# Kernel optimization log

Hardware: AMD Instinct MI355X
Metric: run time of the kernel (lower is better)

## Reference

```python
import jax, jax.numpy as jnp
import numpy as np

DEPTH = 8            # max(code_depth)
CODE_DEPTH = (1, 8)  # (vqgan_depth, vqkd_depth)
N_EMBED = 8192
EMBED_DIM = 64
B, H, W = 32, 32, 32


def setup_inputs() -> dict:
    key = jax.random.key(0)
    kx, kc = jax.random.split(key)
    x = jax.random.normal(kx, (B, EMBED_DIM, H, W), dtype=jnp.float32)
    # 8 codebooks, each (n_embed, embed_dim); torch nn.Embedding init is N(0,1)
    codebooks = jax.random.normal(kc, (DEPTH, N_EMBED, EMBED_DIM), dtype=jnp.float32)
    return {"x": x, "codebooks": codebooks}


def _quantize(x_code, codebooks):
    # x_code: (B, h, w, d) -- already stop-gradient'd (torch clones a detached copy)
    b, h, w, d = x_code.shape
    xf = x_code.reshape(-1, d)  # (N, d)

    def step(carry, cb):
        residual, agg = carry
        # squared L2 distances via ||r||^2 + ||c||^2 - 2 r c^T  (torch addmm)
        r_sq = jnp.sum(residual * residual, axis=1, keepdims=True)      # (N, 1)
        c_sq = jnp.sum(cb * cb, axis=1)[None, :]                         # (1, K)
        dist = r_sq + c_sq - 2.0 * (residual @ cb.T)                     # (N, K)
        code = jnp.argmin(dist, axis=1)                                  # (N,)
        quant = cb[code]                                                 # (N, d)
        d_norm = jnp.mean(jnp.sum(dist * dist, axis=-1))
        residual = residual - quant
        agg = agg + quant
        return (residual, agg), (agg, code, d_norm)

    (_, _), (quants, codes, d_norms) = jax.lax.scan(
        step, (xf, jnp.zeros_like(xf)), codebooks)
    quants = quants.reshape(DEPTH, b, h, w, d)             # cumulative quants
    codes = jnp.transpose(codes.reshape(DEPTH, b, h, w), (1, 2, 3, 0))  # (B,h,w,DEPTH)
    return quants, codes, d_norms


def reference(x, codebooks):
    x_code = jnp.transpose(x, (0, 2, 3, 1))  # b c h w -> b h w c
    quants, codes, d_norms = _quantize(jax.lax.stop_gradient(x_code), codebooks)
    # commitment loss: mean over depth of mean((x - agg_quant.detach())^2)
    commit_loss = jnp.mean((x_code[None] - jax.lax.stop_gradient(quants)) ** 2)
    # straight-through outputs in latent (b c h w) shape
    vqkd = jnp.transpose(quants[CODE_DEPTH[1] - 1], (0, 3, 1, 2))
    vqkd_zq = x + jax.lax.stop_gradient(vqkd - x)
    vqgan = jnp.transpose(quants[CODE_DEPTH[0] - 1], (0, 3, 1, 2))
    vqgan_zq = x + jax.lax.stop_gradient(vqgan - x)
    vqkd_d_norm = d_norms[CODE_DEPTH[1] - 1]
    vqgan_d_norm = d_norms[CODE_DEPTH[0] - 1]
    return (vqgan_zq, vqkd_zq, commit_loss, vqkd_d_norm, vqgan_d_norm, codes)
```

## Files before the change

kernel.cpp:

```cpp
#include <hip/hip_runtime.h>

#define OFF_RES    0u
#define OFF_BH     8388608u
#define OFF_BL     9437184u
#define OFF_CSQD   10485760u
#define OFF_CSQH   11010048u
#define OFF_CODES  11272192u
#define OFF_PM1    11403264u
#define OFF_PM2    12451840u
#define OFF_PI1    13500416u
#define OFF_FLAG   14548992u
#define OFF_M0     14680064u
#define OFF_M7     14712832u
#define OFF_DNP    14745600u
#define OFF_ACC    14749696u
#define OFF_PCOM   14749760u
#define OFF_PDN    15274048u

#define TAU 3.0e-3f

typedef __attribute__((ext_vector_type(8))) _Float16 f16x8;
typedef __attribute__((ext_vector_type(4))) float f32x4;

__device__ __forceinline__ f32x4 mfma16(f16x8 a, f16x8 b, f32x4 c) {
  return __builtin_amdgcn_mfma_f32_16x16x32_f16(a, b, c, 0, 0, 0);
}

__global__ __launch_bounds__(256) void srq_transpose_init(
    const float* __restrict__ x, float* __restrict__ resid)
{
  __shared__ float tile[64][65];
  const int b   = blockIdx.x >> 4;
  const int hw0 = (blockIdx.x & 15) << 6;
  const int t = threadIdx.x;
#pragma unroll
  for (int i = 0; i < 16; ++i) {
    int e = i * 256 + t;
    int c = e >> 6, hw = e & 63;
    tile[c][hw] = x[(size_t)b * 65536 + (size_t)c * 1024 + hw0 + hw];
  }
  __syncthreads();
#pragma unroll
  for (int i = 0; i < 16; ++i) {
    int e = i * 256 + t;
    int hw = e >> 6, c = e & 63;
    resid[((size_t)(b * 1024 + hw0 + hw) << 6) + c] = tile[c][hw];
  }
}

__global__ __launch_bounds__(256) void srq_csq(
    const float* __restrict__ cb, double* __restrict__ csqD, float* __restrict__ csqH)
{
  int id = blockIdx.x * 256 + threadIdx.x;
  const float* p = cb + ((size_t)id << 6);
  double s = 0.0;
#pragma unroll 8
  for (int d = 0; d < 64; ++d) { double v = (double)p[d]; s = fma(v, v, s); }
  csqD[id] = s;
  csqH[id] = (float)(-0.5 * s);
}

__global__ __launch_bounds__(256) void srq_bconv(
    const float* __restrict__ cb, _Float16* __restrict__ Bh, _Float16* __restrict__ Bl)
{
  int id = blockIdx.x * 256 + threadIdx.x;
  float v = cb[id];
  _Float16 h = (_Float16)v;
  Bh[id] = h;
  Bl[id] = (_Float16)((v - (float)h) * 2048.f);
}

__global__ __launch_bounds__(256) void srq_dnpre_partial(
    const float* __restrict__ cb, const double* __restrict__ csqD,
    double* __restrict__ Pm, double* __restrict__ Ps1, double* __restrict__ Ps2)
{
  __shared__ float ch[32][64];
  const int t = threadIdx.x;
  const int b = blockIdx.x;
  const int i = t >> 2;
  const int j0 = (t & 3) << 4;
  double acc[16];
#pragma unroll
  for (int n = 0; n < 16; ++n) acc[n] = 0.0;
  double s1 = 0.0, s2 = 0.0;
  for (int c8 = 0; c8 < 8; ++c8) {
    const int kbase = b * 256 + c8 * 32;
    __syncthreads();
    const float* src = cb + (size_t)kbase * 64;
#pragma unroll
    for (int u = 0; u < 2; ++u)
      *(float4*)(&ch[0][0] + (u * 256 + t) * 4) = *(const float4*)(src + (u * 256 + t) * 4);
    __syncthreads();
#pragma unroll 4
    for (int kk = 0; kk < 32; ++kk) {
      double ci = (double)ch[kk][i];
#pragma unroll
      for (int n = 0; n < 16; ++n)
        acc[n] = fma(ci, (double)ch[kk][j0 + n], acc[n]);
    }
    if (t < 64) {
#pragma unroll 4
      for (int kk = 0; kk < 32; ++kk) {
        double v = (double)ch[kk][t];
        s1 += v;
        s2 = fma(csqD[kbase + kk], v, s2);
      }
    }
  }
  double* dst = Pm + ((size_t)b << 12) + (i << 6) + j0;
#pragma unroll
  for (int n = 0; n < 16; ++n) dst[n] = acc[n];
  if (t < 64) { Ps1[(b << 6) + t] = s1; Ps2[(b << 6) + t] = s2; }
}

__global__ __launch_bounds__(256) void srq_dnpre_reduce(
    const double* __restrict__ Pm, const double* __restrict__ Ps1,
    const double* __restrict__ Ps2, const double* __restrict__ csqD,
    double* __restrict__ Mmat, double* __restrict__ S1, double* __restrict__ S2,
    double* __restrict__ CS)
{
  const int t = threadIdx.x;
  if (blockIdx.x < 16) {
    const int e = blockIdx.x * 256 + t;
    double a = 0.0;
    for (int b = 0; b < 32; ++b) a += Pm[((size_t)b << 12) + e];
    Mmat[e] = a;
  } else {
    __shared__ double red[256];
    if (t < 64) {
      double a1 = 0.0, a2 = 0.0;
      for (int b = 0; b < 32; ++b) { a1 += Ps1[(b << 6) + t]; a2 += Ps2[(b << 6) + t]; }
      S1[t] = a1; S2[t] = a2;
    }
    double c1 = 0.0, c2 = 0.0;
    for (int k = t; k < 8192; k += 256) { double q = csqD[k]; c1 += q; c2 = fma(q, q, c2); }
    red[t] = c1;
    __syncthreads();
    for (int o = 128; o; o >>= 1) { if (t < o) red[t] += red[t + o]; __syncthreads(); }
    if (t == 0) CS[0] = red[0];
    __syncthreads();
    red[t] = c2;
    __syncthreads();
    for (int o = 128; o; o >>= 1) { if (t < o) red[t] += red[t + o]; __syncthreads(); }
    if (t == 0) CS[1] = red[0];
  }
}

__device__ __forceinline__ void stage_tile(
    const _Float16* __restrict__ Bh, const _Float16* __restrict__ Bl,
    char* ldsbase, int k0, int wid, int lane)
{
#pragma unroll
  for (int q = 0; q < 4; ++q) {
    int ub = (((q << 2) + wid) << 10);
    int db = ub + lane * 16;
    int half = db >> 13;
    int rowh = (db & 8191) >> 7;
    int soff = (db & 127) ^ ((rowh & 7) << 4);
    const _Float16* g = (half ? Bl : Bh) + (((size_t)(k0 + rowh)) << 6) + (soff >> 1);
    __builtin_amdgcn_global_load_lds(
        (const __attribute__((address_space(1))) void*)g,
        (__attribute__((address_space(3))) void*)(ldsbase + ub), 16, 0, 0);
  }
}

__global__ __launch_bounds__(256, 3) void srq_screen_mfma(
    const _Float16* __restrict__ Bh, const _Float16* __restrict__ Bl,
    const float* __restrict__ csqH, const float* __restrict__ resid,
    float* __restrict__ pm1, float* __restrict__ pm2, int* __restrict__ pi1)
{
  __shared__ char lds[32768];
  const int tid = threadIdx.x;
  const int lane = tid & 63;
  const int wid = tid >> 6;
  const int rg = blockIdx.x & 255;
  const int ks = blockIdx.x >> 8;
  const int k0g = ks << 10;
  const int wrow0 = (rg << 7) + (wid << 5);
  const int lr = lane & 15;
  const int kg = lane >> 4;

  f16x8 ah[2][2], al[2][2];
#pragma unroll
  for (int rf = 0; rf < 2; ++rf)
#pragma unroll
    for (int s = 0; s < 2; ++s) {
      const float* rp = resid + (((size_t)(wrow0 + rf * 16 + lr)) << 6) + s * 32 + kg * 8;
      float4 v0 = *(const float4*)rp;
      float4 v1 = *(const float4*)(rp + 4);
      float f[8] = {v0.x, v0.y, v0.z, v0.w, v1.x, v1.y, v1.z, v1.w};
      f16x8 h, l;
#pragma unroll
      for (int e = 0; e < 8; ++e) {
        _Float16 hh = (_Float16)f[e];
        h[e] = hh;
        l[e] = (_Float16)((f[e] - (float)hh) * 2048.f);
      }
      ah[rf][s] = h;
      al[rf][s] = l;
    }

  float m1[8], m2[8];
  int i1[8];
#pragma unroll
  for (int j = 0; j < 8; ++j) { m1[j] = -3e38f; m2[j] = -3e38f; i1[j] = 0; }

  stage_tile(Bh, Bl, lds, k0g, wid, lane);

  for (int t = 0; t < 16; ++t) {
    __syncthreads();
    if (t < 15) stage_tile(Bh, Bl, lds + (((t + 1) & 1) << 14), k0g + ((t + 1) << 6), wid, lane);
    const char* bb = lds + ((t & 1) << 14);
    const int k0 = k0g + (t << 6);
#pragma unroll
    for (int cf = 0; cf < 4; ++cf) {
      const int cl = cf * 16 + lr;
      const int sw = (cl & 7) << 4;
      const int ro = cl * 128 + kg * 16;
      f16x8 bh0 = *(const f16x8*)(bb + ((ro) ^ sw));
      f16x8 bh1 = *(const f16x8*)(bb + ((ro + 64) ^ sw));
      f16x8 bl0 = *(const f16x8*)(bb + 8192 + ((ro) ^ sw));
      f16x8 bl1 = *(const f16x8*)(bb + 8192 + ((ro + 64) ^ sw));
      const int code = k0 + cl;
      const float ci = csqH[code];
#pragma unroll
      for (int rf = 0; rf < 2; ++rf) {
        f32x4 a1 = {ci, ci, ci, ci};
        f32x4 a2 = {0.f, 0.f, 0.f, 0.f};
        a1 = mfma16(ah[rf][0], bh0, a1);
        a1 = mfma16(ah[rf][1], bh1, a1);
        a2 = mfma16(ah[rf][0], bl0, a2);
        a2 = mfma16(al[rf][0], bh0, a2);
        a2 = mfma16(ah[rf][1], bl1, a2);
        a2 = mfma16(al[rf][1], bh1, a2);
#pragma unroll
        for (int r = 0; r < 4; ++r) {
          float sg = fmaf(4.8828125e-4f, a2[r], a1[r]);
          const int j = rf * 4 + r;
          bool gt = sg > m1[j];
          m2[j] = __builtin_amdgcn_fmed3f(sg, m1[j], m2[j]);
          m1[j] = fmaxf(m1[j], sg);
          i1[j] = gt ? code : i1[j];
        }
      }
    }
  }

#pragma unroll
  for (int j = 0; j < 8; ++j) {
    float a1 = m1[j], a2 = m2[j];
    int ai = i1[j];
#pragma unroll
    for (int w = 1; w <= 8; w <<= 1) {
      float b1 = __shfl_xor(a1, w);
      float b2 = __shfl_xor(a2, w);
      int bi = __shfl_xor(ai, w);
      float nm2 = fmaxf(fminf(a1, b1), fmaxf(a2, b2));
      bool bet = (b1 > a1) || (b1 == a1 && bi < ai);
      a1 = fmaxf(a1, b1);
      ai = bet ? bi : ai;
      a2 = nm2;
    }
    if (lr == 0) {
      const int row = wrow0 + (j >> 2) * 16 + kg * 4 + (j & 3);
      pm1[row * 8 + ks] = -2.f * a1;
      pm2[row * 8 + ks] = -2.f * a2;
      pi1[row * 8 + ks] = ai;
    }
  }
}

template <int NEED_DN>
__global__ __launch_bounds__(256) void srq_merge_update(
    const float* __restrict__ pm1, const float* __restrict__ pm2,
    const int* __restrict__ pi1, const float* __restrict__ cb,
    float* __restrict__ resid, int* __restrict__ codes, float* __restrict__ codesF,
    int* __restrict__ flagList, int* __restrict__ flagCnt,
    double* __restrict__ Pcom, double* __restrict__ Pdn,
    const double* __restrict__ Mmat, const double* __restrict__ S1v,
    const double* __restrict__ S2v, const double* __restrict__ CS, int dep)
{
  __shared__ double w4[4];
  __shared__ double dnW[4];
  __shared__ float rstage[4][64];
  const int t = threadIdx.x;
  const int team = t >> 6;
  const int c = t & 63;
  const int row = blockIdx.x * 4 + team;

  float m1 = pm1[row * 8], m2 = pm2[row * 8];
  int i1 = pi1[row * 8];
#pragma unroll
  for (int k = 1; k < 8; ++k) {
    float b1 = pm1[row * 8 + k], b2 = pm2[row * 8 + k];
    int bi = pi1[row * 8 + k];
    m2 = fminf(fmaxf(m1, b1), fminf(m2, b2));
    if (b1 < m1) { m1 = b1; i1 = bi; }
  }
  const int code = i1;
  const bool ok = (m2 - m1) >= TAU;

  const size_t ri = ((size_t)row << 6) + c;
  const float rpre = resid[ri];

  if (NEED_DN) {
    rstage[team][c] = rpre;
    __syncthreads();
    const double rc = (double)rpre;
    double mr = 0.0;
#pragma unroll 4
    for (int i = 0; i < 64; ++i)
      mr = fma(Mmat[i * 64 + c], (double)rstage[team][i], mr);
    double qm = mr * rc;
    double av = rc * S1v[c];
    double b2 = rc * S2v[c];
    double r2 = rc * rc;
#pragma unroll
    for (int o = 32; o; o >>= 1) {
      qm += __shfl_down(qm, o);
      av += __shfl_down(av, o);
      b2 += __shfl_down(b2, o);
      r2 += __shfl_down(r2, o);
    }
    if (c == 0) {
      dnW[team] = 8192.0 * r2 * r2 + CS[1] + 4.0 * qm
                + 2.0 * r2 * CS[0] - 4.0 * r2 * av - 4.0 * b2;
    }
  }

  float p = 0.f;
  if (ok) {
    float q = cb[((size_t)code << 6) + c];
    float r = rpre - q;
    resid[ri] = r;
    p = r * r;
  }
#pragma unroll
  for (int o = 32; o; o >>= 1) p += __shfl_down(p, o);
  if (c == 0) {
    codes[row] = code;
    codesF[(size_t)row * 8 + dep] = (float)code;
    w4[team] = (double)p;
    if (!ok) {
      int pos = atomicAdd(flagCnt, 1);
      flagList[pos] = row;
    }
  }
  __syncthreads();
  if (t == 0) Pcom[blockIdx.x] = (w4[0] + w4[1]) + (w4[2] + w4[3]);
  if (NEED_DN && t == 1) Pdn[blockIdx.x] = (dnW[0] + dnW[1]) + (dnW[2] + dnW[3]);
}

__global__ __launch_bounds__(256) void srq_refine(
    const float* __restrict__ cb, const double* __restrict__ csqD,
    float* __restrict__ resid, int* __restrict__ codes,
    const int* __restrict__ flagList, const int* __restrict__ flagCnt,
    float* __restrict__ codesF, double* __restrict__ commitAcc, int dep)
{
  __shared__ float rowv[64];
  __shared__ double vals[256];
  __shared__ int   idxs[256];
  __shared__ int   sbest;
  int cnt = *flagCnt;
  for (int j = blockIdx.x; j < cnt; j += gridDim.x) {
    int row = flagList[j];
    __syncthreads();
    if (threadIdx.x < 64) rowv[threadIdx.x] = resid[((size_t)row << 6) + threadIdx.x];
    __syncthreads();
    double bv = 1e300;
    int bi = 0x7fffffff;
    for (int i = 0; i < 32; ++i) {
      int k = i * 256 + threadIdx.x;
      const float* cp = cb + ((size_t)k << 6);
      double a0 = 0.0, a1 = 0.0, a2 = 0.0, a3 = 0.0;
#pragma unroll
      for (int d = 0; d < 64; d += 4) {
        a0 = fma((double)rowv[d    ], (double)cp[d    ], a0);
        a1 = fma((double)rowv[d + 1], (double)cp[d + 1], a1);
        a2 = fma((double)rowv[d + 2], (double)cp[d + 2], a2);
        a3 = fma((double)rowv[d + 3], (double)cp[d + 3], a3);
      }
      double s = csqD[k] - 2.0 * ((a0 + a1) + (a2 + a3));
      if (s < bv) { bv = s; bi = k; }
    }
    vals[threadIdx.x] = bv;
    idxs[threadIdx.x] = bi;
    __syncthreads();
    if (threadIdx.x == 0) {
      double g = vals[0]; int gi = idxs[0];
      for (int u = 1; u < 256; ++u) {
        if (vals[u] < g || (vals[u] == g && idxs[u] < gi)) { g = vals[u]; gi = idxs[u]; }
      }
      codes[row] = gi;
      codesF[(size_t)row * 8 + dep] = (float)gi;
      sbest = gi;
    }
    __syncthreads();
    if (threadIdx.x < 64) {
      int code = sbest;
      float q = cb[((size_t)code << 6) + threadIdx.x];
      float r = rowv[threadIdx.x] - q;
      resid[((size_t)row << 6) + threadIdx.x] = r;
      float p = r * r;
#pragma unroll
      for (int o = 32; o; o >>= 1) p += __shfl_down(p, o);
      if (threadIdx.x == 0) atomicAdd(commitAcc, (double)p);
    }
  }
}

__global__ __launch_bounds__(256) void srq_writeout(
    const float* __restrict__ x, const float* __restrict__ resid, float* __restrict__ out)
{
  __shared__ float tile[64][65];
  const int b   = blockIdx.x >> 4;
  const int hw0 = (blockIdx.x & 15) << 6;
  const int t = threadIdx.x;
#pragma unroll
  for (int i = 0; i < 16; ++i) {
    int e = i * 256 + t;
    int hw = e >> 6, c = e & 63;
    tile[hw][c] = resid[((size_t)(b * 1024 + hw0 + hw) << 6) + c];
  }
  __syncthreads();
#pragma unroll
  for (int i = 0; i < 16; ++i) {
    int e = i * 256 + t;
    int c = e >> 6, hw = e & 63;
    size_t o = (size_t)b * 65536 + (size_t)c * 1024 + hw0 + hw;
    out[o] = x[o] - tile[hw][c];
  }
}

__global__ __launch_bounds__(256) void srq_finalize(
    const double* __restrict__ Pcom, const double* __restrict__ Pdn,
    const double* __restrict__ acc, float* __restrict__ outs)
{
  __shared__ double red[256];
  const int t = threadIdx.x;
  double s = 0.0;
  for (int i = t; i < 65536; i += 256) s += Pcom[i];
  red[t] = s;
  __syncthreads();
  for (int o = 128; o; o >>= 1) { if (t < o) red[t] += red[t + o]; __syncthreads(); }
  const double commit = red[0] + acc[0];
  __syncthreads();
  s = 0.0;
  for (int i = t; i < 8192; i += 256) s += Pdn[i];
  red[t] = s;
  __syncthreads();
  for (int o = 128; o; o >>= 1) { if (t < o) red[t] += red[t + o]; __syncthreads(); }
  const double dn0 = red[0];
  __syncthreads();
  s = 0.0;
  for (int i = t; i < 8192; i += 256) s += Pdn[8192 + i];
  red[t] = s;
  __syncthreads();
  for (int o = 128; o; o >>= 1) { if (t < o) red[t] += red[t + o]; __syncthreads(); }
  if (t == 0) {
    outs[0] = (float)(commit / 16777216.0);
    outs[1] = (float)(red[0] / 32768.0);
    outs[2] = (float)(dn0 / 32768.0);
  }
}

extern "C" void kernel_launch(void* const* d_in, const int* in_sizes, int n_in,
                              void* d_out, int out_size, void* d_ws, size_t ws_size,
                              hipStream_t stream) {
  const float* x  = (const float*)d_in[0];
  const float* cb = (const float*)d_in[1];
  char* ws = (char*)d_ws;

  float*  resid = (float*)(ws + OFF_RES);
  _Float16* Bh  = (_Float16*)(ws + OFF_BH);
  _Float16* Bl  = (_Float16*)(ws + OFF_BL);
  double* csqD  = (double*)(ws + OFF_CSQD);
  float*  csqH  = (float*)(ws + OFF_CSQH);
  int*    codes = (int*)(ws + OFF_CODES);
  float*  pm1   = (float*)(ws + OFF_PM1);
  float*  pm2   = (float*)(ws + OFF_PM2);
  int*    pi1   = (int*)(ws + OFF_PI1);
  int*    flags = (int*)(ws + OFF_FLAG);
  double* M0    = (double*)(ws + OFF_M0);
  double* M7    = (double*)(ws + OFF_M7);
  double* S1_0  = (double*)(ws + OFF_DNP);
  double* S2_0  = (double*)(ws + OFF_DNP + 512);
  double* S1_7  = (double*)(ws + OFF_DNP + 1024);
  double* S2_7  = (double*)(ws + OFF_DNP + 1536);
  double* CS0   = (double*)(ws + OFF_DNP + 2048);
  double* CS7   = (double*)(ws + OFF_DNP + 2064);
  double* acc   = (double*)(ws + OFF_ACC);
  int*    fcnt  = (int*)(ws + OFF_ACC + 24);
  double* Pcom  = (double*)(ws + OFF_PCOM);
  double* Pdn   = (double*)(ws + OFF_PDN);

  double* Pm  = (double*)(ws + OFF_PM1);
  double* Ps1 = (double*)(ws + OFF_PM2);
  double* Ps2 = (double*)(ws + OFF_PI1);

  float* out_vqgan = (float*)d_out;
  float* out_vqkd  = out_vqgan + 2097152;
  float* out_scal  = out_vqgan + 4194304;
  float* out_codes = out_vqgan + 4194307;

  hipMemsetAsync(ws + OFF_ACC, 0, 56, stream);
  srq_transpose_init<<<512, 256, 0, stream>>>(x, resid);
  srq_csq<<<256, 256, 0, stream>>>(cb, csqD, csqH);
  srq_dnpre_partial<<<32, 256, 0, stream>>>(cb, csqD, Pm, Ps1, Ps2);
  srq_dnpre_reduce<<<17, 256, 0, stream>>>(Pm, Ps1, Ps2, csqD, M0, S1_0, S2_0, CS0);
  srq_dnpre_partial<<<32, 256, 0, stream>>>(cb + (size_t)7 * 524288, csqD + 7 * 8192,
                                            Pm, Ps1, Ps2);
  srq_dnpre_reduce<<<17, 256, 0, stream>>>(Pm, Ps1, Ps2, csqD + 7 * 8192,
                                           M7, S1_7, S2_7, CS7);

  for (int dep = 0; dep < 8; ++dep) {
    const float* cbd = cb + (size_t)dep * 524288;
    srq_bconv<<<2048, 256, 0, stream>>>(cbd, Bh, Bl);
    srq_screen_mfma<<<2048, 256, 0, stream>>>(Bh, Bl, csqH + dep * 8192, resid, pm1, pm2, pi1);
    if (dep == 0 || dep == 7) {
      srq_merge_update<1><<<8192, 256, 0, stream>>>(pm1, pm2, pi1, cbd,
          resid, codes, out_codes, flags, fcnt + dep,
          Pcom + (size_t)dep * 8192, Pdn + (dep == 0 ? 0 : 8192),
          (dep == 0 ? M0 : M7), (dep == 0 ? S1_0 : S1_7),
          (dep == 0 ? S2_0 : S2_7), (dep == 0 ? CS0 : CS7), dep);
    } else {
      srq_merge_update<0><<<8192, 256, 0, stream>>>(pm1, pm2, pi1, cbd,
          resid, codes, out_codes, flags, fcnt + dep,
          Pcom + (size_t)dep * 8192, nullptr,
          nullptr, nullptr, nullptr, nullptr, dep);
    }
    srq_refine<<<128, 256, 0, stream>>>(cbd, csqD + dep * 8192, resid, codes,
                                        flags, fcnt + dep, out_codes, acc, dep);
    if (dep == 0) srq_writeout<<<512, 256, 0, stream>>>(x, resid, out_vqgan);
    if (dep == 7) srq_writeout<<<512, 256, 0, stream>>>(x, resid, out_vqkd);
  }
  srq_finalize<<<1, 256, 0, stream>>>(Pcom, Pdn, acc, out_scal);
}
```

Baseline: 1.972 ms.

## Fuse exact refine and next-codebook fp16 conversion into merge_update kernel

Removes the separate srq_refine kernel, its atomic flag list and its commit accumulator. Flagged rows now get the exact fp64 rescan inside merge_update, where the whole 256-thread block searches each team's row. The fp16 hi/lo conversion of the next depth's codebook also moves into merge_update, which drops the per-depth bconv launch. Screen launch bounds go from 3 to 4 waves. The cost is that a block with any flagged row stalls its other teams through the full 8192-code scan, so blocks become imbalanced and occupancy may drop.

```diff
diff --git a/kernel.cpp b/kernel.cpp
--- a/kernel.cpp
+++ b/kernel.cpp
@@ -9,7 +9,6 @@
 #define OFF_PM1    11403264u
 #define OFF_PM2    12451840u
 #define OFF_PI1    13500416u
-#define OFF_FLAG   14548992u
 #define OFF_M0     14680064u
 #define OFF_M7     14712832u
 #define OFF_DNP    14745600u
@@ -164,7 +163,7 @@
   }
 }
 
-__global__ __launch_bounds__(256, 3) void srq_screen_mfma(
+__global__ __launch_bounds__(256, 4) void srq_screen_mfma(
     const _Float16* __restrict__ Bh, const _Float16* __restrict__ Bl,
     const float* __restrict__ csqH, const float* __restrict__ resid,
     float* __restrict__ pm1, float* __restrict__ pm2, int* __restrict__ pi1)
@@ -274,19 +273,35 @@
 __global__ __launch_bounds__(256) void srq_merge_update(
     const float* __restrict__ pm1, const float* __restrict__ pm2,
     const int* __restrict__ pi1, const float* __restrict__ cb,
+    const double* __restrict__ csqD,
     float* __restrict__ resid, int* __restrict__ codes, float* __restrict__ codesF,
-    int* __restrict__ flagList, int* __restrict__ flagCnt,
     double* __restrict__ Pcom, double* __restrict__ Pdn,
     const double* __restrict__ Mmat, const double* __restrict__ S1v,
-    const double* __restrict__ S2v, const double* __restrict__ CS, int dep)
-{
+    const double* __restrict__ S2v, const double* __restrict__ CS,
+    const float* __restrict__ cbNext, _Float16* __restrict__ BhN,
+    _Float16* __restrict__ BlN, int dep)
+{
+  __shared__ float  rstage[4][64];
   __shared__ double w4[4];
   __shared__ double dnW[4];
-  __shared__ float rstage[4][64];
+  __shared__ int    sflag[4];
+  __shared__ int    sbest[4];
+  __shared__ double vals[256];
+  __shared__ int    idxs[256];
   const int t = threadIdx.x;
   const int team = t >> 6;
   const int c = t & 63;
   const int row = blockIdx.x * 4 + team;
+
+  if (cbNext) {
+    int gid = blockIdx.x * 256 + t;
+    if (gid < 524288) {
+      float v = cbNext[gid];
+      _Float16 h = (_Float16)v;
+      BhN[gid] = h;
+      BlN[gid] = (_Float16)((v - (float)h) * 2048.f);
+    }
+  }
 
   float m1 = pm1[row * 8], m2 = pm2[row * 8];
   int i1 = pi1[row * 8];
@@ -297,15 +312,15 @@
     m2 = fminf(fmaxf(m1, b1), fminf(m2, b2));
     if (b1 < m1) { m1 = b1; i1 = bi; }
   }
-  const int code = i1;
   const bool ok = (m2 - m1) >= TAU;
 
   const size_t ri = ((size_t)row << 6) + c;
   const float rpre = resid[ri];
+  rstage[team][c] = rpre;
+  if (c == 0) sflag[team] = ok ? -1 : 1;
+  __syncthreads();
 
   if (NEED_DN) {
-    rstage[team][c] = rpre;
-    __syncthreads();
     const double rc = (double)rpre;
     double mr = 0.0;
 #pragma unroll 4
@@ -328,85 +343,55 @@
     }
   }
 
-  float p = 0.f;
-  if (ok) {
-    float q = cb[((size_t)code << 6) + c];
-    float r = rpre - q;
-    resid[ri] = r;
-    p = r * r;
-  }
+#pragma unroll 1
+  for (int tm = 0; tm < 4; ++tm) {
+    if (sflag[tm] != -1) {
+      double bv = 1e300;
+      int bi = 0x7fffffff;
+#pragma unroll 1
+      for (int i = 0; i < 32; ++i) {
+        int k = i * 256 + t;
+        const float* cp = cb + ((size_t)k << 6);
+        double a0 = 0.0, a1d = 0.0, a2d = 0.0, a3d = 0.0;
+#pragma unroll
+        for (int d = 0; d < 64; d += 4) {
+          a0  = fma((double)rstage[tm][d    ], (double)cp[d    ], a0);
+          a1d = fma((double)rstage[tm][d + 1], (double)cp[d + 1], a1d);
+          a2d = fma((double)rstage[tm][d + 2], (double)cp[d + 2], a2d);
+          a3d = fma((double)rstage[tm][d + 3], (double)cp[d + 3], a3d);
+        }
+        double s = csqD[k] - 2.0 * ((a0 + a1d) + (a2d + a3d));
+        if (s < bv) { bv = s; bi = k; }
+      }
+      vals[t] = bv;
+      idxs[t] = bi;
+      __syncthreads();
+      if (t == 0) {
+        double g = vals[0]; int gi = idxs[0];
+        for (int u = 1; u < 256; ++u) {
+          if (vals[u] < g || (vals[u] == g && idxs[u] < gi)) { g = vals[u]; gi = idxs[u]; }
+        }
+        sbest[tm] = gi;
+      }
+      __syncthreads();
+    }
+  }
+
+  const int codeF = (sflag[team] == -1) ? i1 : sbest[team];
+  float q = cb[((size_t)codeF << 6) + c];
+  float r = rpre - q;
+  resid[ri] = r;
+  float p = r * r;
 #pragma unroll
   for (int o = 32; o; o >>= 1) p += __shfl_down(p, o);
   if (c == 0) {
-    codes[row] = code;
-    codesF[(size_t)row * 8 + dep] = (float)code;
+    codes[row] = codeF;
+    codesF[(size_t)row * 8 + dep] = (float)codeF;
     w4[team] = (double)p;
-    if (!ok) {
-      int pos = atomicAdd(flagCnt, 1);
-      flagList[pos] = row;
-    }
   }
   __syncthreads();
   if (t == 0) Pcom[blockIdx.x] = (w4[0] + w4[1]) + (w4[2] + w4[3]);
   if (NEED_DN && t == 1) Pdn[blockIdx.x] = (dnW[0] + dnW[1]) + (dnW[2] + dnW[3]);
-}
-
-__global__ __launch_bounds__(256) void srq_refine(
-    const float* __restrict__ cb, const double* __restrict__ csqD,
-    float* __restrict__ resid, int* __restrict__ codes,
-    const int* __restrict__ flagList, const int* __restrict__ flagCnt,
-    float* __restrict__ codesF, double* __restrict__ commitAcc, int dep)
-{
-  __shared__ float rowv[64];
-  __shared__ double vals[256];
-  __shared__ int   idxs[256];
-  __shared__ int   sbest;
-  int cnt = *flagCnt;
-  for (int j = blockIdx.x; j < cnt; j += gridDim.x) {
-    int row = flagList[j];
-    __syncthreads();
-    if (threadIdx.x < 64) rowv[threadIdx.x] = resid[((size_t)row << 6) + threadIdx.x];
-    __syncthreads();
-    double bv = 1e300;
-    int bi = 0x7fffffff;
-    for (int i = 0; i < 32; ++i) {
-      int k = i * 256 + threadIdx.x;
-      const float* cp = cb + ((size_t)k << 6);
-      double a0 = 0.0, a1 = 0.0, a2 = 0.0, a3 = 0.0;
-#pragma unroll
-      for (int d = 0; d < 64; d += 4) {
-        a0 = fma((double)rowv[d    ], (double)cp[d    ], a0);
-        a1 = fma((double)rowv[d + 1], (double)cp[d + 1], a1);
-        a2 = fma((double)rowv[d + 2], (double)cp[d + 2], a2);
-        a3 = fma((double)rowv[d + 3], (double)cp[d + 3], a3);
-      }
-      double s = csqD[k] - 2.0 * ((a0 + a1) + (a2 + a3));
-      if (s < bv) { bv = s; bi = k; }
-    }
-    vals[threadIdx.x] = bv;
-    idxs[threadIdx.x] = bi;
-    __syncthreads();
-    if (threadIdx.x == 0) {
-      double g = vals[0]; int gi = idxs[0];
-      for (int u = 1; u < 256; ++u) {
-        if (vals[u] < g || (vals[u] == g && idxs[u] < gi)) { g = vals[u]; gi = idxs[u]; }
-      }
-      codes[row] = gi;
-      codesF[(size_t)row * 8 + dep] = (float)gi;
-      sbest = gi;
-    }
-    __syncthreads();
-    if (threadIdx.x < 64) {
-      int code = sbest;
-      float q = cb[((size_t)code << 6) + threadIdx.x];
-      float r = rowv[threadIdx.x] - q;
-      resid[((size_t)row << 6) + threadIdx.x] = r;
-      float p = r * r;
-#pragma unroll
-      for (int o = 32; o; o >>= 1) p += __shfl_down(p, o);
-      if (threadIdx.x == 0) atomicAdd(commitAcc, (double)p);
-    }
-  }
 }
 
 __global__ __launch_bounds__(256) void srq_writeout(
@@ -434,7 +419,7 @@
 
 __global__ __launch_bounds__(256) void srq_finalize(
     const double* __restrict__ Pcom, const double* __restrict__ Pdn,
-    const double* __restrict__ acc, float* __restrict__ outs)
+    float* __restrict__ outs)
 {
   __shared__ double red[256];
   const int t = threadIdx.x;
@@ -443,7 +428,7 @@
   red[t] = s;
   __syncthreads();
   for (int o = 128; o; o >>= 1) { if (t < o) red[t] += red[t + o]; __syncthreads(); }
-  const double commit = red[0] + acc[0];
+  const double commit = red[0];
   __syncthreads();
   s = 0.0;
   for (int i = t; i < 8192; i += 256) s += Pdn[i];
@@ -480,7 +465,6 @@
   float*  pm1   = (float*)(ws + OFF_PM1);
   float*  pm2   = (float*)(ws + OFF_PM2);
   int*    pi1   = (int*)(ws + OFF_PI1);
-  int*    flags = (int*)(ws + OFF_FLAG);
   double* M0    = (double*)(ws + OFF_M0);
   double* M7    = (double*)(ws + OFF_M7);
   double* S1_0  = (double*)(ws + OFF_DNP);
@@ -489,8 +473,6 @@
   double* S2_7  = (double*)(ws + OFF_DNP + 1536);
   double* CS0   = (double*)(ws + OFF_DNP + 2048);
   double* CS7   = (double*)(ws + OFF_DNP + 2064);
-  double* acc   = (double*)(ws + OFF_ACC);
-  int*    fcnt  = (int*)(ws + OFF_ACC + 24);
   double* Pcom  = (double*)(ws + OFF_PCOM);
   double* Pdn   = (double*)(ws + OFF_PDN);
 
@@ -503,7 +485,6 @@
   float* out_scal  = out_vqgan + 4194304;
   float* out_codes = out_vqgan + 4194307;
 
-  hipMemsetAsync(ws + OFF_ACC, 0, 56, stream);
   srq_transpose_init<<<512, 256, 0, stream>>>(x, resid);
   srq_csq<<<256, 256, 0, stream>>>(cb, csqD, csqH);
   srq_dnpre_partial<<<32, 256, 0, stream>>>(cb, csqD, Pm, Ps1, Ps2);
@@ -512,27 +493,28 @@
                                             Pm, Ps1, Ps2);
   srq_dnpre_reduce<<<17, 256, 0, stream>>>(Pm, Ps1, Ps2, csqD + 7 * 8192,
                                            M7, S1_7, S2_7, CS7);
+  srq_bconv<<<2048, 256, 0, stream>>>(cb, Bh, Bl);
 
   for (int dep = 0; dep < 8; ++dep) {
     const float* cbd = cb + (size_t)dep * 524288;
-    srq_bconv<<<2048, 256, 0, stream>>>(cbd, Bh, Bl);
+    const float* cbn = (dep < 7) ? cb + (size_t)(dep + 1) * 524288 : nullptr;
     srq_screen_mfma<<<2048, 256, 0, stream>>>(Bh, Bl, csqH + dep * 8192, resid, pm1, pm2, pi1);
     if (dep == 0 || dep == 7) {
       srq_merge_update<1><<<8192, 256, 0, stream>>>(pm1, pm2, pi1, cbd,
-          resid, codes, out_codes, flags, fcnt + dep,
+          csqD + dep * 8192, resid, codes, out_codes,
           Pcom + (size_t)dep * 8192, Pdn + (dep == 0 ? 0 : 8192),
           (dep == 0 ? M0 : M7), (dep == 0 ? S1_0 : S1_7),
-          (dep == 0 ? S2_0 : S2_7), (dep == 0 ? CS0 : CS7), dep);
+          (dep == 0 ? S2_0 : S2_7), (dep == 0 ? CS0 : CS7),
+          cbn, Bh, Bl, dep);
     } else {
       srq_merge_update<0><<<8192, 256, 0, stream>>>(pm1, pm2, pi1, cbd,
-          resid, codes, out_codes, flags, fcnt + dep,
+          csqD + dep * 8192, resid, codes, out_codes,
           Pcom + (size_t)dep * 8192, nullptr,
-          nullptr, nullptr, nullptr, nullptr, dep);
-    }
-    srq_refine<<<128, 256, 0, stream>>>(cbd, csqD + dep * 8192, resid, codes,
-                                        flags, fcnt + dep, out_codes, acc, dep);
+          nullptr, nullptr, nullptr, nullptr,
+          cbn, Bh, Bl, dep);
+    }
     if (dep == 0) srq_writeout<<<512, 256, 0, stream>>>(x, resid, out_vqgan);
     if (dep == 7) srq_writeout<<<512, 256, 0, stream>>>(x, resid, out_vqkd);
   }
-  srq_finalize<<<1, 256, 0, stream>>>(Pcom, Pdn, acc, out_scal);
-}
+  srq_finalize<<<1, 256, 0, stream>>>(Pcom, Pdn, out_scal);
+}
```

After: 4.395 ms. +122.8%, slower.
